# Optimization experiments

Measured on AMD Instinct MI355X. Metric: run time of the kernel, lower is better.

The kernel has to match this reference:

```python
import jax, jax.numpy as jnp
import numpy as np

N = 50000
E = 1600000
IN, HID, OUT = 32, 64, 64

def setup_inputs() -> dict:
    key = jax.random.key(0)
    ks = jax.random.split(key, 10)
    x1 = jax.random.normal(ks[0], (N, IN), dtype=jnp.float32)
    x2 = jax.random.normal(ks[1], (N, IN), dtype=jnp.float32)
    ei1 = jax.random.randint(ks[2], (2, E), 0, N, dtype=jnp.int64)
    ei2 = jax.random.randint(ks[3], (2, E), 0, N, dtype=jnp.int64)
    s1 = 1.0 / np.sqrt(2 * IN)
    s2 = 1.0 / np.sqrt(2 * HID)
    W1 = jax.random.uniform(ks[4], (2 * IN, HID), jnp.float32, -s1, s1)
    b1 = jax.random.uniform(ks[5], (HID,), jnp.float32, -s1, s1)
    prelu_a = jnp.full((HID,), 0.25, dtype=jnp.float32)  # PReLU per-channel init
    W2 = jax.random.uniform(ks[6], (2 * HID, OUT), jnp.float32, -s2, s2)
    b2 = jax.random.uniform(ks[7], (OUT,), jnp.float32, -s2, s2)
    return {"x1": x1, "edge_index1": ei1, "x2": x2, "edge_index2": ei2,
            "W1": W1, "b1": b1, "prelu_a": prelu_a, "W2": W2, "b2": b2}

def _edge_conv(x, src, dst, W, b, n_nodes):
    # PyG EdgeConv: msg = MLP([x_i, x_j - x_i]), aggr = max over incoming edges
    xi = x[dst]                     # [E, d] target node feats
    xj = x[src]                     # [E, d] source node feats
    msg = jax.nn.relu(jnp.concatenate([xi, xj - xi], axis=-1) @ W + b)  # [E, out]
    agg = jax.ops.segment_max(msg, dst, num_segments=n_nodes)
    return jnp.where(jnp.isfinite(agg), agg, 0.0)  # nodes with no in-edges -> 0

def _prelu(x, a):
    return jnp.where(x >= 0, x, a * x)

def _embed(x, edge_index, W1, b1, prelu_a, W2, b2):
    src, dst = edge_index[0], edge_index[1]
    h = _prelu(_edge_conv(x, src, dst, W1, b1, x.shape[0]), prelu_a)
    return _edge_conv(h, src, dst, W2, b2, x.shape[0])

def reference(x1, edge_index1, x2, edge_index2, W1, b1, prelu_a, W2, b2):
    e1 = _embed(x1, edge_index1, W1, b1, prelu_a, W2, b2)
    e2 = _embed(x2, edge_index2, W1, b1, prelu_a, W2, b2)
    return (e1, e2)
```

## Files before the change

### kernel.cpp

```cpp
#include <hip/hip_runtime.h>
#include <hip/hip_fp16.h>


constexpr int HID   = 64;
constexpr int TILE  = 64;
constexpr int TSH   = 6;
constexpr int CAP   = 2560;
constexpr int MAXNB = 1024;
constexpr int EPT   = 4;
constexpr int CAPN  = 96;

typedef _Float16 half8 __attribute__((ext_vector_type(8)));
typedef float    f32x4 __attribute__((ext_vector_type(4)));

__device__ __forceinline__ unsigned int pkmax(unsigned int a, unsigned int b) {
    unsigned int d;
    asm("v_pk_max_f16 %0, %1, %2" : "=v"(d) : "v"(a), "v"(b));
    return d;
}
__device__ __forceinline__ unsigned int f2hbits(float f) {
    const __half h = __float2half_rn(f);
    return (unsigned int)*reinterpret_cast<const unsigned short*>(&h);
}
__device__ __forceinline__ float h2f(unsigned int b16) {
    const unsigned short b = (unsigned short)b16;
    __half h;
    *reinterpret_cast<unsigned short*>(&h) = b;
    return __half2float(h);
}

struct G {
    const float* x;
    const int*   src;
    const int*   dst;
    int* bcnt;
    unsigned int* bin;
    float*          u;
    unsigned short* vk;
    _Float16*       h;
    float*          out;
};

__global__ __launch_bounds__(256) void prep_w_kernel(
    const float* __restrict__ W1, const float* __restrict__ W2,
    _Float16* __restrict__ Wc1, _Float16* __restrict__ Wc2,
    unsigned short* __restrict__ vkS0, unsigned short* __restrict__ vkS1, int N)
{
    const int i = blockIdx.x * 256 + threadIdx.x;
    if (i < 32 * 64) {
        const int k = i >> 6, c = i & 63;
        const float lo = W1[k * 64 + c], hi = W1[(32 + k) * 64 + c];
        Wc1[k * 128 + c]      = (_Float16)(lo - hi);
        Wc1[k * 128 + 64 + c] = (_Float16)hi;
    }
    const int j = i - 32 * 64;
    if (j >= 0 && j < 64 * 64) {
        const int k = j >> 6, c = j & 63;
        const float lo = W2[k * 64 + c], hi = W2[(64 + k) * 64 + c];
        Wc2[k * 128 + c]      = (_Float16)(lo - hi);
        Wc2[k * 128 + 64 + c] = (_Float16)hi;
    }
    const int q = i - (32 * 64 + 64 * 64);
    if (q >= 0 && q < 2 * HID) {
        if (q < HID) vkS0[(size_t)N * HID + q]       = 0xFC00u;
        else         vkS1[(size_t)N * HID + (q-HID)] = 0xFC00u;
    }
}

__global__ __launch_bounds__(1024) void bin_kernel(G g0, G g1, int E, int NB) {
    const G g = blockIdx.y ? g1 : g0;
    __shared__ int lh[MAXNB];
    __shared__ int lb[MAXNB];
    for (int i = threadIdx.x; i < NB; i += 1024) lh[i] = 0;
    __syncthreads();

    const int base = blockIdx.x * 1024 * EPT;
    unsigned int rec[EPT];
    int bb[EPT];
    #pragma unroll
    for (int k = 0; k < EPT; ++k) {
        const int i = base + k * 1024 + threadIdx.x;
        if (i < E) {
            const int d = g.dst[i];
            const int s = g.src[i];
            rec[k] = ((unsigned int)s << TSH) | (unsigned int)(d & (TILE - 1));
            bb[k]  = d >> TSH;
            atomicAdd(&lh[bb[k]], 1);
        } else bb[k] = -1;
    }
    __syncthreads();
    for (int t = threadIdx.x; t < NB; t += 1024) {
        const int c = lh[t];
        lb[t] = c ? atomicAdd(&g.bcnt[t], c) : 0;
        lh[t] = 0;
    }
    __syncthreads();
    #pragma unroll
    for (int k = 0; k < EPT; ++k) {
        if (bb[k] >= 0) {
            const int off = atomicAdd(&lh[bb[k]], 1);
            const int pos = lb[bb[k]] + off;
            if (pos < CAP)
                g.bin[(size_t)bb[k] * CAP + pos] = rec[k];
        }
    }
}

template<int K, bool IN16>
__global__ __launch_bounds__(256) void gemm_mfma_kernel(
    G g0, G g1, const _Float16* __restrict__ Wc,
    const float* __restrict__ bias, int N)
{
    const G g = blockIdx.y ? g1 : g0;
    constexpr int KH = K / 32;
    const int lane = threadIdx.x & 63;
    const int m    = lane & 15;
    const int quad = lane >> 4;
    const int wid  = (blockIdx.x * 256 + threadIdx.x) >> 6;
    const int nW   = (gridDim.x * 256) >> 6;

    half8 bf[8][KH];
    #pragma unroll
    for (int t = 0; t < 8; ++t)
        #pragma unroll
        for (int hh = 0; hh < KH; ++hh)
            #pragma unroll
            for (int j = 0; j < 8; ++j)
                bf[t][hh][j] = Wc[(hh * 32 + quad * 8 + j) * 128 + t * 16 + m];

    float bv[4];
    #pragma unroll
    for (int t = 0; t < 4; ++t) bv[t] = bias[t * 16 + m];

    const int tiles = (N + 15) / 16;

    for (int tile = wid; tile < tiles; tile += nW) {
        const int nbase = tile * 16;
        const int nodeA = min(nbase + m, N - 1);

        half8 a[KH];
        if constexpr (IN16) {
            const half8* rp = (const half8*)(g.h + (size_t)nodeA * K);
            #pragma unroll
            for (int hh = 0; hh < KH; ++hh) a[hh] = rp[hh * 4 + quad];
        } else {
            const float4* rp = (const float4*)(g.x + (size_t)nodeA * K);
            #pragma unroll
            for (int hh = 0; hh < KH; ++hh) {
                const float4 f0 = rp[hh * 8 + quad * 2];
                const float4 f1 = rp[hh * 8 + quad * 2 + 1];
                a[hh][0] = (_Float16)f0.x; a[hh][1] = (_Float16)f0.y;
                a[hh][2] = (_Float16)f0.z; a[hh][3] = (_Float16)f0.w;
                a[hh][4] = (_Float16)f1.x; a[hh][5] = (_Float16)f1.y;
                a[hh][6] = (_Float16)f1.z; a[hh][7] = (_Float16)f1.w;
            }
        }

        f32x4 acc[8];
        #pragma unroll
        for (int t = 0; t < 8; ++t) {
            acc[t] = (f32x4){0.f, 0.f, 0.f, 0.f};
            #pragma unroll
            for (int hh = 0; hh < KH; ++hh)
                acc[t] = __builtin_amdgcn_mfma_f32_16x16x32_f16(
                    a[hh], bf[t][hh], acc[t], 0, 0, 0);
        }

        #pragma unroll
        for (int r = 0; r < 4; ++r) {
            const int node = nbase + quad * 4 + r;
            if (node < N) {
                float* urow = g.u + (size_t)node * HID;
                #pragma unroll
                for (int t = 0; t < 4; ++t)
                    urow[t * 16 + m] = acc[t][r] + bv[t];
                const unsigned int e0 = f2hbits(acc[4][r]);
                const unsigned int e1 = f2hbits(acc[5][r]);
                const unsigned int e2 = f2hbits(acc[6][r]);
                const unsigned int e3 = f2hbits(acc[7][r]);
                uint2 pack;
                pack.x = (e1 << 16) | e0;
                pack.y = (e3 << 16) | e2;
                ((uint2*)(g.vk + (size_t)node * HID))[m] = pack;
            }
        }
    }
}

template<bool OUT16>
__global__ __launch_bounds__(256) void agg_kernel(G g0, G g1, int N, int NB, int two) {
    int b, gi;
    if (two) {
        const int bid = blockIdx.x;
        const int xcd = bid & 7;
        gi = xcd >> 2;
        b  = (bid >> 3) * 4 + (xcd & 3);
    } else { gi = 0; b = blockIdx.x; }
    if (b >= NB) return;
    const G g = gi ? g1 : g0;

    __shared__ int lcnt[TILE];
    __shared__ alignas(16) unsigned short lrec[TILE][CAPN];
    for (int i = threadIdx.x; i < TILE; i += 256) lcnt[i] = 0;
    __syncthreads();

    const int cnt = min(g.bcnt[b], CAP);
    const unsigned int* __restrict__ bp = g.bin + (size_t)b * CAP;
    for (int i = threadIdx.x; i < cnt; i += 256) {
        const unsigned int rec = bp[i];
        const int d = rec & (TILE - 1);
        const int p = atomicAdd(&lcnt[d], 1);
        if (p < CAPN) lrec[d][p] = (unsigned short)(rec >> TSH);
    }
    __syncthreads();
    for (int t = threadIdx.x; t < TILE; t += 256) {
        const int c  = min(lcnt[t], CAPN);
        const int cp = (c + 15) & ~15;
        for (int p = c; p < cp; ++p) lrec[t][p] = (unsigned short)N;
        lcnt[t] = cp;
    }
    __syncthreads();

    const int grp = threadIdx.x >> 4;
    const int sub = threadIdx.x & 15;
    const uint2* __restrict__ vk2 = (const uint2*)g.vk;

    #pragma unroll
    for (int i = 0; i < 4; ++i) {
        const int nl = grp + 16 * i;
        const int n  = b * TILE + nl;
        if (n >= N) continue;
        const int cp = lcnt[nl];

        unsigned int m0 = 0xFC00FC00u, m1 = 0xFC00FC00u;
        for (int j = 0; j < cp; j += 16) {
            const uint4 q0 = *(const uint4*)(&lrec[nl][j]);
            const uint4 q1 = *(const uint4*)(&lrec[nl][j + 8]);
            unsigned int s[16];
            s[0]  = q0.x & 0xFFFFu; s[1]  = q0.x >> 16;
            s[2]  = q0.y & 0xFFFFu; s[3]  = q0.y >> 16;
            s[4]  = q0.z & 0xFFFFu; s[5]  = q0.z >> 16;
            s[6]  = q0.w & 0xFFFFu; s[7]  = q0.w >> 16;
            s[8]  = q1.x & 0xFFFFu; s[9]  = q1.x >> 16;
            s[10] = q1.y & 0xFFFFu; s[11] = q1.y >> 16;
            s[12] = q1.z & 0xFFFFu; s[13] = q1.z >> 16;
            s[14] = q1.w & 0xFFFFu; s[15] = q1.w >> 16;
            uint2 a[16];
            #pragma unroll
            for (int k = 0; k < 16; ++k) a[k] = vk2[(size_t)s[k] * 16 + sub];
            #pragma unroll
            for (int k = 0; k < 16; ++k) {
                m0 = pkmax(m0, a[k].x);
                m1 = pkmax(m1, a[k].y);
            }
        }

        const bool has = cp > 0;
        const float* __restrict__ urow = g.u + (size_t)n * HID;
        const float r0 = has ? fmaxf(urow[sub]      + h2f(m0 & 0xFFFFu), 0.f) : 0.f;
        const float r1 = has ? fmaxf(urow[sub + 16] + h2f(m0 >> 16),     0.f) : 0.f;
        const float r2 = has ? fmaxf(urow[sub + 32] + h2f(m1 & 0xFFFFu), 0.f) : 0.f;
        const float r3 = has ? fmaxf(urow[sub + 48] + h2f(m1 >> 16),     0.f) : 0.f;
        if constexpr (OUT16) {
            _Float16* hrow = g.h + (size_t)n * HID;
            hrow[sub]      = (_Float16)r0;
            hrow[sub + 16] = (_Float16)r1;
            hrow[sub + 32] = (_Float16)r2;
            hrow[sub + 48] = (_Float16)r3;
        } else {
            float* __restrict__ orow = g.out + (size_t)n * HID;
            orow[sub]      = r0;
            orow[sub + 16] = r1;
            orow[sub + 32] = r2;
            orow[sub + 48] = r3;
        }
    }
}


extern "C" void kernel_launch(void* const* d_in, const int* in_sizes, int n_in,
                              void* d_out, int out_size, void* d_ws, size_t ws_size,
                              hipStream_t stream) {
    const float* x1  = (const float*)d_in[0];
    const int*   ei1 = (const int*)d_in[1];
    const float* x2  = (const float*)d_in[2];
    const int*   ei2 = (const int*)d_in[3];
    const float* W1  = (const float*)d_in[4];
    const float* b1  = (const float*)d_in[5];
    const float* W2  = (const float*)d_in[7];
    const float* b2  = (const float*)d_in[8];

    const int N  = in_sizes[0] / 32;
    const int E  = in_sizes[1] / 2;
    const int NB = (N + TILE - 1) / TILE;
    float* out = (float*)d_out;

    const size_t rowB = (size_t)N * HID * sizeof(float);
    const size_t vkB  = ((size_t)(N + 1) * HID * 2 + 63) & ~(size_t)63;
    const size_t hB   = ((size_t)N * HID * 2 + 63) & ~(size_t)63;
    const size_t binB = ((size_t)NB * CAP * sizeof(int) + 63) & ~(size_t)63;
    const size_t nbB  = ((size_t)(NB + 2) * sizeof(int) + 63) & ~(size_t)63;
    const size_t wc1B = ((size_t)32 * 128 * 2 + 63) & ~(size_t)63;
    const size_t wc2B = ((size_t)64 * 128 * 2 + 63) & ~(size_t)63;

    const int bBlk = (E + 1024 * EPT - 1) / (1024 * EPT);
    const int gBlk = 512;
    const int pBlk = (32 * 64 + 64 * 64 + 2 * HID + 255) / 256;
    const int aggBlk2 = ((NB + 3) / 4) * 8;
    const int aggBlk1 = NB;

    _Float16* wc1 = nullptr;
    _Float16* wc2 = nullptr;

    auto run = [&](G ga, G gb, int ny) {
        hipMemsetAsync(ga.bcnt, 0, (size_t)ny * nbB, stream);
        bin_kernel <<<dim3(bBlk, ny), 1024, 0, stream>>>(ga, gb, E, NB);
        gemm_mfma_kernel<32,false><<<dim3(gBlk, ny), 256, 0, stream>>>(ga, gb, wc1, b1, N);
        if (ny == 2) agg_kernel<true><<<aggBlk2, 256, 0, stream>>>(ga, gb, N, NB, 1);
        else         agg_kernel<true><<<aggBlk1, 256, 0, stream>>>(ga, ga, N, NB, 0);
        gemm_mfma_kernel<64,true><<<dim3(gBlk, ny), 256, 0, stream>>>(ga, gb, wc2, b2, N);
        if (ny == 2) agg_kernel<false><<<aggBlk2, 256, 0, stream>>>(ga, gb, N, NB, 1);
        else         agg_kernel<false><<<aggBlk1, 256, 0, stream>>>(ga, ga, N, NB, 0);
    };

    char* ws = (char*)d_ws;
    const size_t needBoth =
        2 * rowB + 2 * binB + 2 * vkB + 2 * hB + wc1B + wc2B + 2 * nbB;

    if (ws_size >= needBoth) {
        float* u0 = (float*)ws;                  ws += rowB;
        float* u1 = (float*)ws;                  ws += rowB;
        unsigned int* bin0 = (unsigned int*)ws;  ws += binB;
        unsigned int* bin1 = (unsigned int*)ws;  ws += binB;
        unsigned short* vk0 = (unsigned short*)ws;  ws += vkB;
        unsigned short* vk1 = (unsigned short*)ws;  ws += vkB;
        _Float16* h0 = (_Float16*)ws;            ws += hB;
        _Float16* h1 = (_Float16*)ws;            ws += hB;
        wc1 = (_Float16*)ws;                     ws += wc1B;
        wc2 = (_Float16*)ws;                     ws += wc2B;
        int* bcnt0 = (int*)ws;                   ws += nbB;
        int* bcnt1 = (int*)ws;

        G g0{x1, ei1, ei1 + E, bcnt0, bin0, u0, vk0, h0, out};
        G g1{x2, ei2, ei2 + E, bcnt1, bin1, u1, vk1, h1, out + (size_t)N * HID};
        prep_w_kernel<<<pBlk, 256, 0, stream>>>(W1, W2, wc1, wc2, vk0, vk1, N);
        run(g0, g1, 2);
    } else {
        float* u = (float*)ws;                   ws += rowB;
        unsigned int* bin = (unsigned int*)ws;   ws += binB;
        unsigned short* vk = (unsigned short*)ws;  ws += vkB;
        _Float16* h = (_Float16*)ws;             ws += hB;
        wc1 = (_Float16*)ws;                     ws += wc1B;
        wc2 = (_Float16*)ws;                     ws += wc2B;
        int* bcnt = (int*)ws;

        prep_w_kernel<<<pBlk, 256, 0, stream>>>(W1, W2, wc1, wc2, vk, vk, N);
        for (int g = 0; g < 2; ++g) {
            const int* ei = g ? ei2 : ei1;
            G gp{g ? x2 : x1, ei, ei + E, bcnt, bin,
                 u, vk, h, out + (size_t)g * N * HID};
            run(gp, gp, 1);
        }
    }
}
```

Baseline: 252.2 us.

## Split edge aggregation by source parity across XCDs and merge partial maxima

```diff
diff --git a/kernel.cpp b/kernel.cpp
--- a/kernel.cpp
+++ b/kernel.cpp
@@ -3,12 +3,12 @@
 
 
 constexpr int HID   = 64;
-constexpr int TILE  = 64;
-constexpr int TSH   = 6;
+constexpr int TILE  = 128;
+constexpr int TSH   = 7;
 constexpr int CAP   = 2560;
 constexpr int MAXNB = 1024;
 constexpr int EPT   = 4;
-constexpr int CAPN  = 96;
+constexpr int CAPN  = 48;
 
 typedef _Float16 half8 __attribute__((ext_vector_type(8)));
 typedef float    f32x4 __attribute__((ext_vector_type(4)));
@@ -18,9 +18,9 @@
     asm("v_pk_max_f16 %0, %1, %2" : "=v"(d) : "v"(a), "v"(b));
     return d;
 }
-__device__ __forceinline__ unsigned int f2hbits(float f) {
+__device__ __forceinline__ unsigned short f2hbits(float f) {
     const __half h = __float2half_rn(f);
-    return (unsigned int)*reinterpret_cast<const unsigned short*>(&h);
+    return *reinterpret_cast<const unsigned short*>(&h);
 }
 __device__ __forceinline__ float h2f(unsigned int b16) {
     const unsigned short b = (unsigned short)b16;
@@ -37,7 +37,7 @@
     unsigned int* bin;
     float*          u;
     unsigned short* vk;
-    _Float16*       h;
+    unsigned short* q;
     float*          out;
 };
 
@@ -84,7 +84,7 @@
             const int d = g.dst[i];
             const int s = g.src[i];
             rec[k] = ((unsigned int)s << TSH) | (unsigned int)(d & (TILE - 1));
-            bb[k]  = d >> TSH;
+            bb[k]  = ((d >> TSH) << 1) | (s & 1);
             atomicAdd(&lh[bb[k]], 1);
         } else bb[k] = -1;
     }
@@ -106,7 +106,7 @@
     }
 }
 
-template<int K, bool IN16>
+template<int K, int MODE>
 __global__ __launch_bounds__(256) void gemm_mfma_kernel(
     G g0, G g1, const _Float16* __restrict__ Wc,
     const float* __restrict__ bias, int N)
@@ -139,10 +139,21 @@
         const int nodeA = min(nbase + m, N - 1);
 
         half8 a[KH];
-        if constexpr (IN16) {
-            const half8* rp = (const half8*)(g.h + (size_t)nodeA * K);
-            #pragma unroll
-            for (int hh = 0; hh < KH; ++hh) a[hh] = rp[hh * 4 + quad];
+        if constexpr (MODE == 1) {
+            const unsigned short* q0r = g.q + (size_t)nodeA * HID;
+            const unsigned short* q1r = q0r + (size_t)N * HID;
+            #pragma unroll
+            for (int hh = 0; hh < KH; ++hh) {
+                const int cb = hh * 32 + quad * 8;
+                const uint4 a0 = *(const uint4*)(q0r + cb);
+                const uint4 a1 = *(const uint4*)(q1r + cb);
+                uint4 rr;
+                rr.x = pkmax(a0.x, a1.x);
+                rr.y = pkmax(a0.y, a1.y);
+                rr.z = pkmax(a0.z, a1.z);
+                rr.w = pkmax(a0.w, a1.w);
+                a[hh] = *reinterpret_cast<half8*>(&rr);
+            }
         } else {
             const float4* rp = (const float4*)(g.x + (size_t)nodeA * K);
             #pragma unroll
@@ -187,17 +198,19 @@
     }
 }
 
-template<bool OUT16>
-__global__ __launch_bounds__(256) void agg_kernel(G g0, G g1, int N, int NB, int two) {
-    int b, gi;
+template<int QOUT>
+__global__ __launch_bounds__(256) void agg_kernel(G g0, G g1, int N, int NBD, int two) {
+    int dstb, sh, gi;
     if (two) {
         const int bid = blockIdx.x;
         const int xcd = bid & 7;
-        gi = xcd >> 2;
-        b  = (bid >> 3) * 4 + (xcd & 3);
-    } else { gi = 0; b = blockIdx.x; }
-    if (b >= NB) return;
+        gi   = xcd >> 2;
+        sh   = (xcd >> 1) & 1;
+        dstb = (bid >> 3) * 2 + (xcd & 1);
+    } else { gi = 0; dstb = blockIdx.x >> 1; sh = blockIdx.x & 1; }
+    if (dstb >= NBD) return;
     const G g = gi ? g1 : g0;
+    const int b = dstb * 2 + sh;
 
     __shared__ int lcnt[TILE];
     __shared__ alignas(16) unsigned short lrec[TILE][CAPN];
@@ -224,11 +237,12 @@
     const int grp = threadIdx.x >> 4;
     const int sub = threadIdx.x & 15;
     const uint2* __restrict__ vk2 = (const uint2*)g.vk;
-
-    #pragma unroll
-    for (int i = 0; i < 4; ++i) {
+    unsigned short* __restrict__ qh = g.q + (size_t)sh * N * HID;
+
+    #pragma unroll
+    for (int i = 0; i < 8; ++i) {
         const int nl = grp + 16 * i;
-        const int n  = b * TILE + nl;
+        const int n  = dstb * TILE + nl;
         if (n >= N) continue;
         const int cp = lcnt[nl];
 
@@ -255,25 +269,34 @@
             }
         }
 
-        const bool has = cp > 0;
-        const float* __restrict__ urow = g.u + (size_t)n * HID;
-        const float r0 = has ? fmaxf(urow[sub]      + h2f(m0 & 0xFFFFu), 0.f) : 0.f;
-        const float r1 = has ? fmaxf(urow[sub + 16] + h2f(m0 >> 16),     0.f) : 0.f;
-        const float r2 = has ? fmaxf(urow[sub + 32] + h2f(m1 & 0xFFFFu), 0.f) : 0.f;
-        const float r3 = has ? fmaxf(urow[sub + 48] + h2f(m1 >> 16),     0.f) : 0.f;
-        if constexpr (OUT16) {
-            _Float16* hrow = g.h + (size_t)n * HID;
-            hrow[sub]      = (_Float16)r0;
-            hrow[sub + 16] = (_Float16)r1;
-            hrow[sub + 32] = (_Float16)r2;
-            hrow[sub + 48] = (_Float16)r3;
+        unsigned short* prow = qh + (size_t)n * HID;
+        if constexpr (QOUT) {
+            const float* __restrict__ urow = g.u + (size_t)n * HID;
+            prow[sub]      = f2hbits(fmaxf(urow[sub]      + h2f(m0 & 0xFFFFu), 0.f));
+            prow[sub + 16] = f2hbits(fmaxf(urow[sub + 16] + h2f(m0 >> 16),     0.f));
+            prow[sub + 32] = f2hbits(fmaxf(urow[sub + 32] + h2f(m1 & 0xFFFFu), 0.f));
+            prow[sub + 48] = f2hbits(fmaxf(urow[sub + 48] + h2f(m1 >> 16),     0.f));
         } else {
-            float* __restrict__ orow = g.out + (size_t)n * HID;
-            orow[sub]      = r0;
-            orow[sub + 16] = r1;
-            orow[sub + 32] = r2;
-            orow[sub + 48] = r3;
-        }
+            prow[sub]      = (unsigned short)(m0 & 0xFFFFu);
+            prow[sub + 16] = (unsigned short)(m0 >> 16);
+            prow[sub + 32] = (unsigned short)(m1 & 0xFFFFu);
+            prow[sub + 48] = (unsigned short)(m1 >> 16);
+        }
+    }
+}
+
+__global__ __launch_bounds__(256) void merge_kernel(G g0, G g1, int N) {
+    const G g = blockIdx.y ? g1 : g0;
+    const int tot = N * (HID / 2);
+    const unsigned int* __restrict__ p0 = (const unsigned int*)g.q;
+    const unsigned int* __restrict__ p1 = p0 + (size_t)N * (HID / 2);
+    for (int i = blockIdx.x * 256 + threadIdx.x; i < tot; i += gridDim.x * 256) {
+        const unsigned int mm = pkmax(p0[i], p1[i]);
+        const float2 uu = *(const float2*)(g.u + (size_t)i * 2);
+        float2 o;
+        o.x = fmaxf(uu.x + h2f(mm & 0xFFFFu), 0.f);
+        o.y = fmaxf(uu.y + h2f(mm >> 16),     0.f);
+        *(float2*)(g.out + (size_t)i * 2) = o;
     }
 }
 
@@ -290,14 +313,15 @@
     const float* W2  = (const float*)d_in[7];
     const float* b2  = (const float*)d_in[8];
 
-    const int N  = in_sizes[0] / 32;
-    const int E  = in_sizes[1] / 2;
-    const int NB = (N + TILE - 1) / TILE;
+    const int N   = in_sizes[0] / 32;
+    const int E   = in_sizes[1] / 2;
+    const int NBD = (N + TILE - 1) / TILE;
+    const int NB  = 2 * NBD;
     float* out = (float*)d_out;
 
     const size_t rowB = (size_t)N * HID * sizeof(float);
     const size_t vkB  = ((size_t)(N + 1) * HID * 2 + 63) & ~(size_t)63;
-    const size_t hB   = ((size_t)N * HID * 2 + 63) & ~(size_t)63;
+    const size_t qB   = ((size_t)2 * N * HID * 2 + 63) & ~(size_t)63;
     const size_t binB = ((size_t)NB * CAP * sizeof(int) + 63) & ~(size_t)63;
     const size_t nbB  = ((size_t)(NB + 2) * sizeof(int) + 63) & ~(size_t)63;
     const size_t wc1B = ((size_t)32 * 128 * 2 + 63) & ~(size_t)63;
@@ -306,8 +330,9 @@
     const int bBlk = (E + 1024 * EPT - 1) / (1024 * EPT);
     const int gBlk = 512;
     const int pBlk = (32 * 64 + 64 * 64 + 2 * HID + 255) / 256;
-    const int aggBlk2 = ((NB + 3) / 4) * 8;
-    const int aggBlk1 = NB;
+    const int aggBlk2 = ((NBD + 1) / 2) * 8;
+    const int aggBlk1 = 2 * NBD;
+    const int mBlk = 1024;
 
     _Float16* wc1 = nullptr;
     _Float16* wc2 = nullptr;
@@ -315,17 +340,18 @@
     auto run = [&](G ga, G gb, int ny) {
         hipMemsetAsync(ga.bcnt, 0, (size_t)ny * nbB, stream);
         bin_kernel <<<dim3(bBlk, ny), 1024, 0, stream>>>(ga, gb, E, NB);
-        gemm_mfma_kernel<32,false><<<dim3(gBlk, ny), 256, 0, stream>>>(ga, gb, wc1, b1, N);
-        if (ny == 2) agg_kernel<true><<<aggBlk2, 256, 0, stream>>>(ga, gb, N, NB, 1);
-        else         agg_kernel<true><<<aggBlk1, 256, 0, stream>>>(ga, ga, N, NB, 0);
-        gemm_mfma_kernel<64,true><<<dim3(gBlk, ny), 256, 0, stream>>>(ga, gb, wc2, b2, N);
-        if (ny == 2) agg_kernel<false><<<aggBlk2, 256, 0, stream>>>(ga, gb, N, NB, 1);
-        else         agg_kernel<false><<<aggBlk1, 256, 0, stream>>>(ga, ga, N, NB, 0);
+        gemm_mfma_kernel<32,0><<<dim3(gBlk, ny), 256, 0, stream>>>(ga, gb, wc1, b1, N);
+        if (ny == 2) agg_kernel<1><<<aggBlk2, 256, 0, stream>>>(ga, gb, N, NBD, 1);
+        else         agg_kernel<1><<<aggBlk1, 256, 0, stream>>>(ga, ga, N, NBD, 0);
+        gemm_mfma_kernel<64,1><<<dim3(gBlk, ny), 256, 0, stream>>>(ga, gb, wc2, b2, N);
+        if (ny == 2) agg_kernel<0><<<aggBlk2, 256, 0, stream>>>(ga, gb, N, NBD, 1);
+        else         agg_kernel<0><<<aggBlk1, 256, 0, stream>>>(ga, ga, N, NBD, 0);
+        merge_kernel<<<dim3(mBlk, ny), 256, 0, stream>>>(ga, gb, N);
     };
 
     char* ws = (char*)d_ws;
     const size_t needBoth =
-        2 * rowB + 2 * binB + 2 * vkB + 2 * hB + wc1B + wc2B + 2 * nbB;
+        2 * rowB + 2 * binB + 2 * vkB + 2 * qB + wc1B + wc2B + 2 * nbB;
 
     if (ws_size >= needBoth) {
         float* u0 = (float*)ws;                  ws += rowB;
@@ -334,22 +360,22 @@
         unsigned int* bin1 = (unsigned int*)ws;  ws += binB;
         unsigned short* vk0 = (unsigned short*)ws;  ws += vkB;
         unsigned short* vk1 = (unsigned short*)ws;  ws += vkB;
-        _Float16* h0 = (_Float16*)ws;            ws += hB;
-        _Float16* h1 = (_Float16*)ws;            ws += hB;
+        unsigned short* q0 = (unsigned short*)ws;   ws += qB;
+        unsigned short* q1 = (unsigned short*)ws;   ws += qB;
         wc1 = (_Float16*)ws;                     ws += wc1B;
         wc2 = (_Float16*)ws;                     ws += wc2B;
         int* bcnt0 = (int*)ws;                   ws += nbB;
         int* bcnt1 = (int*)ws;
 
-        G g0{x1, ei1, ei1 + E, bcnt0, bin0, u0, vk0, h0, out};
-        G g1{x2, ei2, ei2 + E, bcnt1, bin1, u1, vk1, h1, out + (size_t)N * HID};
+        G g0{x1, ei1, ei1 + E, bcnt0, bin0, u0, vk0, q0, out};
+        G g1{x2, ei2, ei2 + E, bcnt1, bin1, u1, vk1, q1, out + (size_t)N * HID};
         prep_w_kernel<<<pBlk, 256, 0, stream>>>(W1, W2, wc1, wc2, vk0, vk1, N);
         run(g0, g1, 2);
     } else {
         float* u = (float*)ws;                   ws += rowB;
         unsigned int* bin = (unsigned int*)ws;   ws += binB;
         unsigned short* vk = (unsigned short*)ws;  ws += vkB;
-        _Float16* h = (_Float16*)ws;             ws += hB;
+        unsigned short* q = (unsigned short*)ws;   ws += qB;
         wc1 = (_Float16*)ws;                     ws += wc1B;
         wc2 = (_Float16*)ws;                     ws += wc2B;
         int* bcnt = (int*)ws;
@@ -358,7 +384,7 @@
         for (int g = 0; g < 2; ++g) {
             const int* ei = g ? ei2 : ei1;
             G gp{g ? x2 : x1, ei, ei + E, bcnt, bin,
-                 u, vk, h, out + (size_t)g * N * HID};
+                 u, vk, q, out + (size_t)g * N * HID};
             run(gp, gp, 1);
         }
     }
```

New measurement: 281.2 us. 1.12x slower.

## Fuse edge binning with first-layer GEMM and shrink aggregation gather batch

Applied to the files above, without the earlier changes.

```diff
diff --git a/kernel.cpp b/kernel.cpp
--- a/kernel.cpp
+++ b/kernel.cpp
@@ -7,7 +7,7 @@
 constexpr int TSH   = 6;
 constexpr int CAP   = 2560;
 constexpr int MAXNB = 1024;
-constexpr int EPT   = 4;
+constexpr int EPT   = 16;
 constexpr int CAPN  = 96;
 
 typedef _Float16 half8 __attribute__((ext_vector_type(8)));
@@ -18,9 +18,9 @@
     asm("v_pk_max_f16 %0, %1, %2" : "=v"(d) : "v"(a), "v"(b));
     return d;
 }
-__device__ __forceinline__ unsigned int f2hbits(float f) {
+__device__ __forceinline__ unsigned short f2hbits(float f) {
     const __half h = __float2half_rn(f);
-    return (unsigned int)*reinterpret_cast<const unsigned short*>(&h);
+    return *reinterpret_cast<const unsigned short*>(&h);
 }
 __device__ __forceinline__ float h2f(unsigned int b16) {
     const unsigned short b = (unsigned short)b16;
@@ -67,103 +67,92 @@
     }
 }
 
-__global__ __launch_bounds__(1024) void bin_kernel(G g0, G g1, int E, int NB) {
-    const G g = blockIdx.y ? g1 : g0;
-    __shared__ int lh[MAXNB];
-    __shared__ int lb[MAXNB];
-    for (int i = threadIdx.x; i < NB; i += 1024) lh[i] = 0;
-    __syncthreads();
-
-    const int base = blockIdx.x * 1024 * EPT;
-    unsigned int rec[EPT];
-    int bb[EPT];
-    #pragma unroll
-    for (int k = 0; k < EPT; ++k) {
-        const int i = base + k * 1024 + threadIdx.x;
-        if (i < E) {
-            const int d = g.dst[i];
-            const int s = g.src[i];
-            rec[k] = ((unsigned int)s << TSH) | (unsigned int)(d & (TILE - 1));
-            bb[k]  = d >> TSH;
-            atomicAdd(&lh[bb[k]], 1);
-        } else bb[k] = -1;
-    }
-    __syncthreads();
-    for (int t = threadIdx.x; t < NB; t += 1024) {
-        const int c = lh[t];
-        lb[t] = c ? atomicAdd(&g.bcnt[t], c) : 0;
-        lh[t] = 0;
-    }
-    __syncthreads();
-    #pragma unroll
-    for (int k = 0; k < EPT; ++k) {
-        if (bb[k] >= 0) {
-            const int off = atomicAdd(&lh[bb[k]], 1);
-            const int pos = lb[bb[k]] + off;
-            if (pos < CAP)
-                g.bin[(size_t)bb[k] * CAP + pos] = rec[k];
-        }
-    }
-}
-
-template<int K, bool IN16>
-__global__ __launch_bounds__(256) void gemm_mfma_kernel(
-    G g0, G g1, const _Float16* __restrict__ Wc,
-    const float* __restrict__ bias, int N)
+__global__ __launch_bounds__(256) void bin_gemm32_kernel(
+    G g0, G g1, int E, int NB, int N,
+    const _Float16* __restrict__ Wc, const float* __restrict__ bias, int bBlk)
 {
     const G g = blockIdx.y ? g1 : g0;
-    constexpr int KH = K / 32;
+
+    if ((int)blockIdx.x < bBlk) {
+        __shared__ int lh[MAXNB];
+        __shared__ int lb[MAXNB];
+        for (int i = threadIdx.x; i < NB; i += 256) lh[i] = 0;
+        __syncthreads();
+
+        const int base = blockIdx.x * 256 * EPT;
+        unsigned int rec[EPT];
+        int bb[EPT];
+        #pragma unroll
+        for (int k = 0; k < EPT; ++k) {
+            const int i = base + k * 256 + threadIdx.x;
+            if (i < E) {
+                const int d = g.dst[i];
+                const int s = g.src[i];
+                rec[k] = ((unsigned int)s << TSH) | (unsigned int)(d & (TILE - 1));
+                bb[k]  = d >> TSH;
+                atomicAdd(&lh[bb[k]], 1);
+            } else bb[k] = -1;
+        }
+        __syncthreads();
+        for (int t = threadIdx.x; t < NB; t += 256) {
+            const int c = lh[t];
+            lb[t] = c ? atomicAdd(&g.bcnt[t], c) : 0;
+            lh[t] = 0;
+        }
+        __syncthreads();
+        #pragma unroll
+        for (int k = 0; k < EPT; ++k) {
+            if (bb[k] >= 0) {
+                const int off = atomicAdd(&lh[bb[k]], 1);
+                const int pos = lb[bb[k]] + off;
+                if (pos < CAP)
+                    g.bin[(size_t)bb[k] * CAP + pos] = rec[k];
+            }
+        }
+        return;
+    }
+
+    constexpr int K = 32;
     const int lane = threadIdx.x & 63;
     const int m    = lane & 15;
     const int quad = lane >> 4;
-    const int wid  = (blockIdx.x * 256 + threadIdx.x) >> 6;
-    const int nW   = (gridDim.x * 256) >> 6;
-
-    half8 bf[8][KH];
+    const int bx   = blockIdx.x - bBlk;
+    const int wid  = (bx * 256 + threadIdx.x) >> 6;
+    const int nW   = ((gridDim.x - bBlk) * 256) >> 6;
+
+    half8 bf[8];
     #pragma unroll
     for (int t = 0; t < 8; ++t)
         #pragma unroll
-        for (int hh = 0; hh < KH; ++hh)
-            #pragma unroll
-            for (int j = 0; j < 8; ++j)
-                bf[t][hh][j] = Wc[(hh * 32 + quad * 8 + j) * 128 + t * 16 + m];
+        for (int j = 0; j < 8; ++j)
+            bf[t][j] = Wc[(quad * 8 + j) * 128 + t * 16 + m];
 
     float bv[4];
     #pragma unroll
     for (int t = 0; t < 4; ++t) bv[t] = bias[t * 16 + m];
 
     const int tiles = (N + 15) / 16;
-
     for (int tile = wid; tile < tiles; tile += nW) {
         const int nbase = tile * 16;
         const int nodeA = min(nbase + m, N - 1);
-
-        half8 a[KH];
-        if constexpr (IN16) {
-            const half8* rp = (const half8*)(g.h + (size_t)nodeA * K);
-            #pragma unroll
-            for (int hh = 0; hh < KH; ++hh) a[hh] = rp[hh * 4 + quad];
-        } else {
-            const float4* rp = (const float4*)(g.x + (size_t)nodeA * K);
-            #pragma unroll
-            for (int hh = 0; hh < KH; ++hh) {
-                const float4 f0 = rp[hh * 8 + quad * 2];
-                const float4 f1 = rp[hh * 8 + quad * 2 + 1];
-                a[hh][0] = (_Float16)f0.x; a[hh][1] = (_Float16)f0.y;
-                a[hh][2] = (_Float16)f0.z; a[hh][3] = (_Float16)f0.w;
-                a[hh][4] = (_Float16)f1.x; a[hh][5] = (_Float16)f1.y;
-                a[hh][6] = (_Float16)f1.z; a[hh][7] = (_Float16)f1.w;
-            }
+        const float4* rp = (const float4*)(g.x + (size_t)nodeA * K);
+
+        half8 a;
+        {
+            const float4 f0 = rp[quad * 2];
+            const float4 f1 = rp[quad * 2 + 1];
+            a[0] = (_Float16)f0.x; a[1] = (_Float16)f0.y;
+            a[2] = (_Float16)f0.z; a[3] = (_Float16)f0.w;
+            a[4] = (_Float16)f1.x; a[5] = (_Float16)f1.y;
+            a[6] = (_Float16)f1.z; a[7] = (_Float16)f1.w;
         }
 
         f32x4 acc[8];
         #pragma unroll
         for (int t = 0; t < 8; ++t) {
             acc[t] = (f32x4){0.f, 0.f, 0.f, 0.f};
-            #pragma unroll
-            for (int hh = 0; hh < KH; ++hh)
-                acc[t] = __builtin_amdgcn_mfma_f32_16x16x32_f16(
-                    a[hh], bf[t][hh], acc[t], 0, 0, 0);
+            acc[t] = __builtin_amdgcn_mfma_f32_16x16x32_f16(
+                a, bf[t], acc[t], 0, 0, 0);
         }
 
         #pragma unroll
@@ -187,6 +176,72 @@
     }
 }
 
+__global__ __launch_bounds__(256) void gemm64_kernel(
+    G g0, G g1, const _Float16* __restrict__ Wc,
+    const float* __restrict__ bias, int N)
+{
+    const G g = blockIdx.y ? g1 : g0;
+    constexpr int K = 64, KH = 2;
+    const int lane = threadIdx.x & 63;
+    const int m    = lane & 15;
+    const int quad = lane >> 4;
+    const int wid  = (blockIdx.x * 256 + threadIdx.x) >> 6;
+    const int nW   = (gridDim.x * 256) >> 6;
+
+    half8 bf[8][KH];
+    #pragma unroll
+    for (int t = 0; t < 8; ++t)
+        #pragma unroll
+        for (int hh = 0; hh < KH; ++hh)
+            #pragma unroll
+            for (int j = 0; j < 8; ++j)
+                bf[t][hh][j] = Wc[(hh * 32 + quad * 8 + j) * 128 + t * 16 + m];
+
+    float bv[4];
+    #pragma unroll
+    for (int t = 0; t < 4; ++t) bv[t] = bias[t * 16 + m];
+
+    const int tiles = (N + 15) / 16;
+    for (int tile = wid; tile < tiles; tile += nW) {
+        const int nbase = tile * 16;
+        const int nodeA = min(nbase + m, N - 1);
+        const half8* rp = (const half8*)(g.h + (size_t)nodeA * K);
+
+        half8 a[KH];
+        #pragma unroll
+        for (int hh = 0; hh < KH; ++hh) a[hh] = rp[hh * 4 + quad];
+
+        f32x4 acc[8];
+        #pragma unroll
+        for (int t = 0; t < 8; ++t) {
+            acc[t] = (f32x4){0.f, 0.f, 0.f, 0.f};
+            #pragma unroll
+            for (int hh = 0; hh < KH; ++hh)
+                acc[t] = __builtin_amdgcn_mfma_f32_16x16x32_f16(
+                    a[hh], bf[t][hh], acc[t], 0, 0, 0);
+        }
+
+        #pragma unroll
+        for (int r = 0; r < 4; ++r) {
+            const int node = nbase + quad * 4 + r;
+            if (node < N) {
+                float* urow = g.u + (size_t)node * HID;
+                #pragma unroll
+                for (int t = 0; t < 4; ++t)
+                    urow[t * 16 + m] = acc[t][r] + bv[t];
+                const unsigned int e0 = f2hbits(acc[4][r]);
+                const unsigned int e1 = f2hbits(acc[5][r]);
+                const unsigned int e2 = f2hbits(acc[6][r]);
+                const unsigned int e3 = f2hbits(acc[7][r]);
+                uint2 pack;
+                pack.x = (e1 << 16) | e0;
+                pack.y = (e3 << 16) | e2;
+                ((uint2*)(g.vk + (size_t)node * HID))[m] = pack;
+            }
+        }
+    }
+}
+
 template<bool OUT16>
 __global__ __launch_bounds__(256) void agg_kernel(G g0, G g1, int N, int NB, int two) {
     int b, gi;
@@ -215,7 +270,7 @@
     __syncthreads();
     for (int t = threadIdx.x; t < TILE; t += 256) {
         const int c  = min(lcnt[t], CAPN);
-        const int cp = (c + 15) & ~15;
+        const int cp = (c + 7) & ~7;
         for (int p = c; p < cp; ++p) lrec[t][p] = (unsigned short)N;
         lcnt[t] = cp;
     }
@@ -233,23 +288,18 @@
         const int cp = lcnt[nl];
 
         unsigned int m0 = 0xFC00FC00u, m1 = 0xFC00FC00u;
-        for (int j = 0; j < cp; j += 16) {
-            const uint4 q0 = *(const uint4*)(&lrec[nl][j]);
-            const uint4 q1 = *(const uint4*)(&lrec[nl][j + 8]);
-            unsigned int s[16];
-            s[0]  = q0.x & 0xFFFFu; s[1]  = q0.x >> 16;
-            s[2]  = q0.y & 0xFFFFu; s[3]  = q0.y >> 16;
-            s[4]  = q0.z & 0xFFFFu; s[5]  = q0.z >> 16;
-            s[6]  = q0.w & 0xFFFFu; s[7]  = q0.w >> 16;
-            s[8]  = q1.x & 0xFFFFu; s[9]  = q1.x >> 16;
-            s[10] = q1.y & 0xFFFFu; s[11] = q1.y >> 16;
-            s[12] = q1.z & 0xFFFFu; s[13] = q1.z >> 16;
-            s[14] = q1.w & 0xFFFFu; s[15] = q1.w >> 16;
-            uint2 a[16];
+        for (int j = 0; j < cp; j += 8) {
+            const uint4 rq = *(const uint4*)(&lrec[nl][j]);
+            unsigned int s[8];
+            s[0] = rq.x & 0xFFFFu; s[1] = rq.x >> 16;
+            s[2] = rq.y & 0xFFFFu; s[3] = rq.y >> 16;
+            s[4] = rq.z & 0xFFFFu; s[5] = rq.z >> 16;
+            s[6] = rq.w & 0xFFFFu; s[7] = rq.w >> 16;
+            uint2 a[8];
             #pragma unroll
-            for (int k = 0; k < 16; ++k) a[k] = vk2[(size_t)s[k] * 16 + sub];
+            for (int k = 0; k < 8; ++k) a[k] = vk2[(size_t)s[k] * 16 + sub];
             #pragma unroll
-            for (int k = 0; k < 16; ++k) {
+            for (int k = 0; k < 8; ++k) {
                 m0 = pkmax(m0, a[k].x);
                 m1 = pkmax(m1, a[k].y);
             }
@@ -303,7 +353,7 @@
     const size_t wc1B = ((size_t)32 * 128 * 2 + 63) & ~(size_t)63;
     const size_t wc2B = ((size_t)64 * 128 * 2 + 63) & ~(size_t)63;
 
-    const int bBlk = (E + 1024 * EPT - 1) / (1024 * EPT);
+    const int bBlk = (E + 256 * EPT - 1) / (256 * EPT);
     const int gBlk = 512;
     const int pBlk = (32 * 64 + 64 * 64 + 2 * HID + 255) / 256;
     const int aggBlk2 = ((NB + 3) / 4) * 8;
@@ -314,11 +364,11 @@
 
     auto run = [&](G ga, G gb, int ny) {
         hipMemsetAsync(ga.bcnt, 0, (size_t)ny * nbB, stream);
-        bin_kernel <<<dim3(bBlk, ny), 1024, 0, stream>>>(ga, gb, E, NB);
-        gemm_mfma_kernel<32,false><<<dim3(gBlk, ny), 256, 0, stream>>>(ga, gb, wc1, b1, N);
+        bin_gemm32_kernel<<<dim3(bBlk + gBlk, ny), 256, 0, stream>>>(
+            ga, gb, E, NB, N, wc1, b1, bBlk);
         if (ny == 2) agg_kernel<true><<<aggBlk2, 256, 0, stream>>>(ga, gb, N, NB, 1);
         else         agg_kernel<true><<<aggBlk1, 256, 0, stream>>>(ga, ga, N, NB, 0);
-        gemm_mfma_kernel<64,true><<<dim3(gBlk, ny), 256, 0, stream>>>(ga, gb, wc2, b2, N);
+        gemm64_kernel<<<dim3(gBlk, ny), 256, 0, stream>>>(ga, gb, wc2, b2, N);
         if (ny == 2) agg_kernel<false><<<aggBlk2, 256, 0, stream>>>(ga, gb, N, NB, 1);
         else         agg_kernel<false><<<aggBlk1, 256, 0, stream>>>(ga, ga, N, NB, 0);
     };
```

Result: faster. 245.2 us (-2.8%).
